# Kernel tuning notes

Hardware: AMD Instinct MI355X
Metric: run time of the kernel (lower is better)

The kernel has to match this reference:

```python
import jax, jax.numpy as jnp
import numpy as np

ROPE_FREQ = 100.0

def _rope1d(tok, pos, freq):
    # tok: [B, H, N, D] (D even), pos: [B, N] int positions
    D = tok.shape[-1]
    inv_freq = 1.0 / (freq ** (jnp.arange(0, D, 2, dtype=jnp.float32) / D))  # [D/2]
    ang = pos[:, None, :, None].astype(jnp.float32) * inv_freq  # [B,1,N,D/2]
    cos = jnp.concatenate([jnp.cos(ang), jnp.cos(ang)], axis=-1).astype(tok.dtype)
    sin = jnp.concatenate([jnp.sin(ang), jnp.sin(ang)], axis=-1).astype(tok.dtype)
    x1, x2 = jnp.split(tok, 2, axis=-1)
    rot = jnp.concatenate([-x2, x1], axis=-1)  # rotate_half
    return tok * cos + rot * sin

def _rope2d(tok, pos2d, freq=ROPE_FREQ):
    # tok: [B, H, N, D]; first half of D encodes y (pos2d[...,0]), second half x (pos2d[...,1])
    y, x = jnp.split(tok, 2, axis=-1)
    y = _rope1d(y, pos2d[..., 0], freq)
    x = _rope1d(x, pos2d[..., 1], freq)
    return jnp.concatenate([y, x], axis=-1)

def setup_inputs() -> dict:
    key = jax.random.key(0)
    B, N, D, Hh = 2, 2048, 768, 12
    ks = jax.random.split(key, 8)
    x = jax.random.normal(ks[0], (B, N, D), dtype=jnp.float32)
    pos2d = jax.random.randint(ks[1], (B, N, 2), 0, 64)
    rope_mask = jax.random.randint(ks[2], (B, N), 0, 2).astype(jnp.bool_)
    s = 1.0 / np.sqrt(D)
    qkv_w = jax.random.normal(ks[3], (3 * D, D), dtype=jnp.float32) * s
    qkv_b = jnp.zeros((3 * D,), dtype=jnp.float32)
    proj_w = jax.random.normal(ks[4], (D, D), dtype=jnp.float32) * s
    proj_b = jnp.zeros((D,), dtype=jnp.float32)
    return {"x": x, "qkv_w": qkv_w, "qkv_b": qkv_b, "proj_w": proj_w,
            "proj_b": proj_b, "pos2d": pos2d, "rope_mask": rope_mask}

def reference(x, qkv_w, qkv_b, proj_w, proj_b, pos2d, rope_mask):
    B, N, C = x.shape
    num_heads = 12
    head_dim = C // num_heads
    scale = head_dim ** -0.5
    qkv = x @ qkv_w.T + qkv_b  # [B,N,3C]
    qkv = qkv.reshape(B, N, 3, num_heads, head_dim).transpose(2, 0, 3, 1, 4)
    q, k, v = qkv[0], qkv[1], qkv[2]  # each [B,H,N,hd]
    q_rope = _rope2d(q, pos2d)
    k_rope = _rope2d(k, pos2d)
    mask = rope_mask[:, None, :, None]  # [B,1,N,1]
    q = jnp.where(mask, q_rope, q)
    k = jnp.where(mask, k_rope, k)
    attn = jnp.einsum('bhqd,bhkd->bhqk', q, k) * scale
    attn = jax.nn.softmax(attn, axis=-1)
    out = jnp.einsum('bhqk,bhkd->bhqd', attn, v)
    out = out.transpose(0, 2, 1, 3).reshape(B, N, C)
    out = out @ proj_w.T + proj_b
    return out
```

## Files before the change

kernel.cpp:

```cpp
#include <hip/hip_runtime.h>
#include <stdint.h>

#define B_  2
#define N_  2048
#define C_  768
#define H_  12
#define NT  (B_*N_)
#define C3  (3*C_)

typedef _Float16 h8 __attribute__((ext_vector_type(8)));
typedef _Float16 h4 __attribute__((ext_vector_type(4)));
typedef float    f4 __attribute__((ext_vector_type(4)));
typedef float    f16x __attribute__((ext_vector_type(16)));
typedef uint32_t u4 __attribute__((ext_vector_type(4)));

__device__ __forceinline__ void gload16(const void* g, void* l) {
  __builtin_amdgcn_global_load_lds((const __attribute__((address_space(1))) void*)g,
                                   (__attribute__((address_space(3))) void*)l,
                                   16, 0, 0);
}

__device__ __forceinline__ int xcd_swz(int flat, int nwg) {
  return (flat & 7) * (nwg >> 3) + (flat >> 3);
}

__global__ __launch_bounds__(256) void cvt3(const float* __restrict__ x,
                                            const float* __restrict__ w1,
                                            const float* __restrict__ w2,
                                            _Float16* __restrict__ xo,
                                            _Float16* __restrict__ w1o,
                                            _Float16* __restrict__ w2o) {
  const int NX8  = NT*C_/8;
  const int NW18 = C3*C_/8;
  int c = blockIdx.x*256 + threadIdx.x;
  const float* s; _Float16* d; int off;
  if (c < NX8)            { s = x;  d = xo;  off = c; }
  else if (c < NX8+NW18)  { s = w1; d = w1o; off = c - NX8; }
  else                    { s = w2; d = w2o; off = c - NX8 - NW18; }
  f4 a = *(const f4*)(s + (size_t)off*8);
  f4 b = *(const f4*)(s + (size_t)off*8 + 4);
  h8 o;
#pragma unroll
  for (int j = 0; j < 4; ++j) { o[j] = (_Float16)a[j]; o[j+4] = (_Float16)b[j]; }
  *(h8*)(d + (size_t)off*8) = o;
}

__global__ __launch_bounds__(256) void gemm_qkv(const _Float16* __restrict__ A,
                                                const _Float16* __restrict__ W,
                                                const float* __restrict__ bias,
                                                const int* __restrict__ pos2d,
                                                const void* __restrict__ maskraw,
                                                _Float16* __restrict__ Qd,
                                                _Float16* __restrict__ Kd,
                                                _Float16* __restrict__ Vtd) {
  constexpr int BM = 64, BN = 128, K = C_;
  __shared__ _Float16 Alds[2][BM*64];
  __shared__ _Float16 Wlds[2][BN*64];
  __shared__ int sflags;
  const int tid = threadIdx.x, lane = tid & 63, w = tid >> 6;

  if (tid == 0) sflags = 0;
  __syncthreads();
  const unsigned char* mbytes = (const unsigned char*)maskraw;
  int fl = 0;
#pragma unroll
  for (int k2 = 0; k2 < 16; ++k2) {
    unsigned char v = mbytes[tid*16 + k2];
    if (v == 0x3f) fl |= 1;
    if ((k2 & 3) && v) fl |= 2;
  }
  if (fl) atomicOr(&sflags, fl);

  const int flat = blockIdx.y * gridDim.x + blockIdx.x;
  const int wid  = xcd_swz(flat, gridDim.x * gridDim.y);
  const int bx = wid % gridDim.x, by = wid / gridDim.x;
  const int m0 = by*BM, n0 = bx*BN;
  const int wm = w >> 1, wn = w & 1;
  const int fr = lane & 15, fq = lane >> 4;

  f4 acc[2][4] = {};

  const int srow = tid >> 3;
  const int scol = ((tid & 7) ^ (srow & 7)) * 8;
  const _Float16* Agp0 = A + (size_t)(m0 +      srow)*K + scol;
  const _Float16* Agp1 = A + (size_t)(m0 + 32 + srow)*K + scol;
  const _Float16* Wgp0 = W + (size_t)(n0 +      srow)*K + scol;
  const _Float16* Wgp1 = W + (size_t)(n0 + 32 + srow)*K + scol;
  const _Float16* Wgp2 = W + (size_t)(n0 + 64 + srow)*K + scol;
  const _Float16* Wgp3 = W + (size_t)(n0 + 96 + srow)*K + scol;

  auto GSTAGE = [&](int buf, int kk) {
    gload16(Agp0 + kk, &Alds[buf][(      w*64)*8]);
    gload16(Agp1 + kk, &Alds[buf][(256 + w*64)*8]);
    gload16(Wgp0 + kk, &Wlds[buf][(      w*64)*8]);
    gload16(Wgp1 + kk, &Wlds[buf][(256 + w*64)*8]);
    gload16(Wgp2 + kk, &Wlds[buf][(512 + w*64)*8]);
    gload16(Wgp3 + kk, &Wlds[buf][(768 + w*64)*8]);
  };

  const int xr = (fr & 7) << 3;

  GSTAGE(0, 0);
  int cur = 0;
  for (int kk = 0; kk < K; kk += 64) {
    __syncthreads();
    if (kk + 64 < K) GSTAGE(cur^1, kk + 64);
#pragma unroll
    for (int ks = 0; ks < 2; ++ks) {
      h8 af[2], wf[4];
#pragma unroll
      for (int mt = 0; mt < 2; ++mt)
        af[mt] = *(const h8*)&Alds[cur][(wm*32 + mt*16 + fr)*64 + ((ks*32 + fq*8) ^ xr)];
#pragma unroll
      for (int nt = 0; nt < 4; ++nt)
        wf[nt] = *(const h8*)&Wlds[cur][(wn*64 + nt*16 + fr)*64 + ((ks*32 + fq*8) ^ xr)];
#pragma unroll
      for (int mt = 0; mt < 2; ++mt)
#pragma unroll
        for (int nt = 0; nt < 4; ++nt)
          acc[mt][nt] = __builtin_amdgcn_mfma_f32_16x16x32_f16(af[mt], wf[nt], acc[mt][nt], 0, 0, 0);
    }
    cur ^= 1;
  }

  const int cb   = (n0 >> 6) + wn;
  const int matc = cb / 12;
  const int h    = cb % 12;
  const int mode = (sflags & 1) ? 2 : ((sflags & 2) ? 1 : 0);
  float bv[4];
#pragma unroll
  for (int nt = 0; nt < 4; ++nt) bv[nt] = bias[cb*64 + nt*16 + fr];

  if (matc < 2) {
    const float invf = exp2f((float)fr * -0.4152410118f);
    const float sc = (matc == 0) ? 0.1803368801f : 1.0f;
    _Float16* base = (matc == 0) ? Qd : Kd;
#pragma unroll
    for (int mt = 0; mt < 2; ++mt)
#pragma unroll
      for (int j = 0; j < 4; ++j) {
        const int t = m0 + wm*32 + mt*16 + fq*4 + j;
        const int b = t >> 11, n = t & 2047;
        bool msk;
        if (mode == 1)      msk = mbytes[t] != 0;
        else if (mode == 0) msk = ((const int*)maskraw)[t] != 0;
        else                msk = ((const float*)maskraw)[t] != 0.0f;
        const float py = (float)pos2d[t*2 + 0];
        const float px = (float)pos2d[t*2 + 1];
        float sy, cy, sx, cx;
        __sincosf(py * invf, &sy, &cy);
        __sincosf(px * invf, &sx, &cx);
        const float a0 = acc[mt][0][j] + bv[0], a1 = acc[mt][1][j] + bv[1];
        const float a2 = acc[mt][2][j] + bv[2], a3 = acc[mt][3][j] + bv[3];
        const float r0 = msk ? (a0*cy - a1*sy) : a0;
        const float r1 = msk ? (a1*cy + a0*sy) : a1;
        const float r2 = msk ? (a2*cx - a3*sx) : a2;
        const float r3 = msk ? (a3*cx + a2*sx) : a3;
        _Float16* dst = base + ((size_t)(b*H_ + h)*N_ + n)*64;
        dst[fr]      = (_Float16)(r0 * sc);
        dst[fr + 16] = (_Float16)(r1 * sc);
        dst[fr + 32] = (_Float16)(r2 * sc);
        dst[fr + 48] = (_Float16)(r3 * sc);
      }
  } else {
#pragma unroll
    for (int mt = 0; mt < 2; ++mt)
#pragma unroll
      for (int j = 0; j < 4; ++j) {
        const int t = m0 + wm*32 + mt*16 + fq*4 + j;
        const int b = t >> 11, n = t & 2047;
        _Float16* vb = Vtd + (size_t)(b*H_ + h)*64*N_ + n;
#pragma unroll
        for (int nt = 0; nt < 4; ++nt)
          vb[(size_t)(nt*16 + fr)*N_] = (_Float16)(acc[mt][nt][j] + bv[nt]);
      }
  }
}

template<int BM, int BN>
__global__ __launch_bounds__(256) void gemm_bt(const _Float16* __restrict__ A,
                                               const _Float16* __restrict__ W,
                                               const float* __restrict__ bias,
                                               _Float16* __restrict__ Ch,
                                               float* __restrict__ Cf,
                                               int M, int N, int K) {
  __shared__ _Float16 Alds[2][BM*32];
  __shared__ _Float16 Wlds[2][BN*32];
  const int tid = threadIdx.x, lane = tid & 63, w = tid >> 6;
  const int flat = blockIdx.y * gridDim.x + blockIdx.x;
  const int wid  = xcd_swz(flat, gridDim.x * gridDim.y);
  const int bx = wid % gridDim.x, by = wid / gridDim.x;
  const int m0 = by*BM, n0 = bx*BN;
  const int wm = w >> 1, wn = w & 1;
  const int fr = lane & 15, fq = lane >> 4;
  constexpr int MT = BM/32, NTt = BN/32;
  constexpr int AI = (BM*4)/256, WI = (BN*4)/256;

  f4 acc[MT][NTt] = {};

  const _Float16* Agp[AI];
  const _Float16* Wgp[WI];
#pragma unroll
  for (int i = 0; i < AI; ++i) { int c = i*256 + tid; Agp[i] = A + (size_t)(m0 + (c>>2))*K + (c&3)*8; }
#pragma unroll
  for (int i = 0; i < WI; ++i) { int c = i*256 + tid; Wgp[i] = W + (size_t)(n0 + (c>>2))*K + (c&3)*8; }

  auto GSTAGE = [&](int buf, int kk) {
#pragma unroll
    for (int i = 0; i < AI; ++i) gload16(Agp[i] + kk, &Alds[buf][(i*256 + w*64)*8]);
#pragma unroll
    for (int i = 0; i < WI; ++i) gload16(Wgp[i] + kk, &Wlds[buf][(i*256 + w*64)*8]);
  };

  GSTAGE(0, 0);
  int cur = 0;
  for (int kk = 0; kk < K; kk += 32) {
    __syncthreads();
    if (kk + 32 < K) GSTAGE(cur^1, kk + 32);
    h8 af[MT], wf[NTt];
#pragma unroll
    for (int mt = 0; mt < MT; ++mt)
      af[mt] = *(const h8*)&Alds[cur][(wm*(BM/2) + mt*16 + fr)*32 + fq*8];
#pragma unroll
    for (int nt = 0; nt < NTt; ++nt)
      wf[nt] = *(const h8*)&Wlds[cur][(wn*(BN/2) + nt*16 + fr)*32 + fq*8];
#pragma unroll
    for (int mt = 0; mt < MT; ++mt)
#pragma unroll
      for (int nt = 0; nt < NTt; ++nt)
        acc[mt][nt] = __builtin_amdgcn_mfma_f32_16x16x32_f16(af[mt], wf[nt], acc[mt][nt], 0, 0, 0);
    cur ^= 1;
  }

#pragma unroll
  for (int nt = 0; nt < NTt; ++nt) {
    const int col = n0 + wn*(BN/2) + nt*16 + fr;
    const float bv = bias[col];
#pragma unroll
    for (int mt = 0; mt < MT; ++mt) {
      const int row = m0 + wm*(BM/2) + mt*16 + fq*4;
#pragma unroll
      for (int j = 0; j < 4; ++j) {
        const float v = acc[mt][nt][j] + bv;
        if (Ch) Ch[(size_t)(row+j)*N + col] = (_Float16)v;
        else    Cf[(size_t)(row+j)*N + col] = v;
      }
    }
  }
}

#define KSPLIT 2
__global__ __launch_bounds__(256, 3) void attn(const _Float16* __restrict__ Q,
                                               const _Float16* __restrict__ K,
                                               const _Float16* __restrict__ Vt,
                                               _Float16* __restrict__ Opart,
                                               float* __restrict__ lpart) {
  __shared__ _Float16 Klds[2][64*64];
  __shared__ _Float16 Vlds[2][64*64];
  const int tid = threadIdx.x, lane = tid & 63, w = tid >> 6;
  const int q32 = lane & 31;
  const int hi  = lane >> 5;
  const int flat = blockIdx.x + gridDim.x*(blockIdx.y + gridDim.y*blockIdx.z);
  const int wid  = xcd_swz(flat, 16*24*KSPLIT);
  const int qi = wid & 15;
  const int bh = (wid >> 4) % 24;
  const int z  = wid / (16*24);
  const int q0 = qi * 128;
  const int kb0 = z * (N_/KSPLIT), kb1 = kb0 + N_/KSPLIT;
  const _Float16* Qb = Q  + (size_t)bh*N_*64;
  const _Float16* Kb = K  + (size_t)bh*N_*64;
  const _Float16* Vb = Vt + (size_t)bh*64*N_;

  h8 qf[4];
#pragma unroll
  for (int s = 0; s < 4; ++s)
    qf[s] = *(const h8*)&Qb[(size_t)(q0 + w*32 + q32)*64 + s*16 + hi*8];

  f16x o2[2][2];
#pragma unroll
  for (int par = 0; par < 2; ++par)
#pragma unroll
    for (int dg = 0; dg < 2; ++dg)
#pragma unroll
      for (int r = 0; r < 16; ++r) o2[par][dg][r] = 0.f;
  float l_r = 0.f;

  const int sr_l = lane >> 3;
  const int scsw = ((lane & 7) ^ sr_l) * 8;
#define STAGE(buf, kb)                                                          \
  {                                                                             \
    _Float16* kl = &Klds[buf][(w*64)*8];                                        \
    _Float16* vl = &Vlds[buf][(w*64)*8];                                        \
    int r0 = w*8 + sr_l;                                                        \
    gload16(Kb + (size_t)((kb) + r0)*64 + scsw,      kl);                       \
    gload16(Vb + (size_t)r0*N_ + (kb) + scsw,        vl);                       \
    gload16(Kb + (size_t)((kb) + 32 + r0)*64 + scsw, kl + 256*8);               \
    gload16(Vb + (size_t)(32 + r0)*N_ + (kb) + scsw, vl + 256*8);               \
  }

  STAGE(0, kb0);
  int cur = 0;
  const int xr = (q32 & 7) << 3;

  for (int kb = kb0; kb < kb1; kb += 64) {
    __syncthreads();
    if (kb + 64 < kb1) STAGE(cur^1, kb + 64);

#pragma unroll
    for (int kg = 0; kg < 2; ++kg) {
      f16x st;
#pragma unroll
      for (int r = 0; r < 16; ++r) st[r] = -8.65617025f;
      __builtin_amdgcn_s_setprio(1);
#pragma unroll
      for (int s = 0; s < 4; ++s) {
        h8 kf = *(const h8*)&Klds[cur][(kg*32 + q32)*64 + ((s*16 + hi*8) ^ xr)];
        st = __builtin_amdgcn_mfma_f32_32x32x16_f16(kf, qf[s], st, 0, 0, 0);
      }
      __builtin_amdgcn_s_setprio(0);
      float p[16];
      float lacc = 0.f;
#pragma unroll
      for (int r = 0; r < 16; ++r) {
        p[r] = __builtin_amdgcn_exp2f(st[r]);
        lacc += p[r];
      }
      l_r += lacc;
      uint32_t dd[8];
#pragma unroll
      for (int m = 0; m < 8; ++m)
        dd[m] = __builtin_bit_cast(uint32_t, __builtin_amdgcn_cvt_pkrtz(p[2*m], p[2*m+1]));
#pragma unroll
      for (int s16 = 0; s16 < 2; ++s16) {
        uint32_t e0 = dd[4*s16+0], e2 = dd[4*s16+2];
        asm("v_permlane32_swap_b32 %0, %1" : "+v"(e0), "+v"(e2));
        uint32_t e1 = dd[4*s16+1], e3 = dd[4*s16+3];
        asm("v_permlane32_swap_b32 %0, %1" : "+v"(e1), "+v"(e3));
        u4 bb;
        bb[0] = e0; bb[1] = e1; bb[2] = e2; bb[3] = e3;
        h8 pb = __builtin_bit_cast(h8, bb);
        const int kcol = kg*32 + s16*16 + hi*8;
        __builtin_amdgcn_s_setprio(1);
#pragma unroll
        for (int dg = 0; dg < 2; ++dg) {
          h8 vf = *(const h8*)&Vlds[cur][(dg*32 + q32)*64 + (kcol ^ xr)];
          o2[s16][dg] = __builtin_amdgcn_mfma_f32_32x32x16_f16(vf, pb, o2[s16][dg], 0, 0, 0);
        }
        __builtin_amdgcn_s_setprio(0);
      }
    }
    cur ^= 1;
  }

  l_r += __shfl_xor(l_r, 32);

  _Float16* Ob = Opart + ((size_t)z*24 + bh)*N_*64;
  float*    lb = lpart + ((size_t)z*24 + bh)*N_;
  const int n = q0 + w*32 + q32;
  if (hi == 0) lb[n] = l_r;
#pragma unroll
  for (int dg = 0; dg < 2; ++dg)
#pragma unroll
    for (int rq = 0; rq < 4; ++rq) {
      h4 ov;
#pragma unroll
      for (int j = 0; j < 4; ++j)
        ov[j] = (_Float16)(o2[0][dg][rq*4 + j] + o2[1][dg][rq*4 + j]);
      *(h4*)&Ob[(size_t)n*64 + dg*32 + rq*8 + hi*4] = ov;
    }
}

__global__ __launch_bounds__(256) void combine(const _Float16* __restrict__ Opart,
                                               const float* __restrict__ lpart,
                                               _Float16* __restrict__ AO) {
  const int g  = blockIdx.x*256 + threadIdx.x;
  const int d8 = g & 7;
  const int n  = (g >> 3) & 2047;
  const int bh = g >> 14;
  const int b = bh / H_, h = bh % H_;
  const size_t r  = ((size_t)bh*N_ + n);
  const size_t sp = (size_t)24*N_;
  f4 osum[2] = {};
  float l = 0.f;
#pragma unroll
  for (int z = 0; z < KSPLIT; ++z) {
    h8 oz = *(const h8*)&Opart[(r + z*sp)*64 + d8*8];
#pragma unroll
    for (int j = 0; j < 4; ++j) { osum[0][j] += (float)oz[j]; osum[1][j] += (float)oz[j+4]; }
    l += lpart[r + z*sp];
  }
  const float inv = 1.0f / l;
  h8 rr;
#pragma unroll
  for (int j = 0; j < 4; ++j) {
    rr[j]   = (_Float16)(osum[0][j] * inv);
    rr[j+4] = (_Float16)(osum[1][j] * inv);
  }
  *(h8*)&AO[((size_t)b*N_ + n)*C_ + h*64 + d8*8] = rr;
}

extern "C" void kernel_launch(void* const* d_in, const int* in_sizes, int n_in,
                              void* d_out, int out_size, void* d_ws, size_t ws_size,
                              hipStream_t stream) {
  (void)in_sizes; (void)n_in; (void)out_size; (void)ws_size;
  const float* x      = (const float*)d_in[0];
  const float* qkv_w  = (const float*)d_in[1];
  const float* qkv_b  = (const float*)d_in[2];
  const float* proj_w = (const float*)d_in[3];
  const float* proj_b = (const float*)d_in[4];
  const int*   pos2d  = (const int*)d_in[5];
  const void*  rmask  = d_in[6];
  float* out = (float*)d_out;
  char* ws = (char*)d_ws;

  _Float16* Wqh   = (_Float16*)(ws + 0);
  _Float16* Wph   = (_Float16*)(ws + 3538944);
  _Float16* Kh    = (_Float16*)(ws + 4718592);
  _Float16* Vth   = (_Float16*)(ws + 11010048);
  _Float16* Xh    = (_Float16*)(ws + 17301504);
  _Float16* Qh    = (_Float16*)(ws + 23592960);
  _Float16* Opart = (_Float16*)(ws + 29884416);
  float*    lpart = (float*)(ws + 42467328);
  _Float16* AOh   = (_Float16*)(ws + 43253760);

  cvt3<<<2688, 256, 0, stream>>>(x, qkv_w, proj_w, Xh, Wqh, Wph);
  gemm_qkv<<<dim3(C3/128, NT/64), 256, 0, stream>>>(Xh, Wqh, qkv_b, pos2d, rmask, Qh, Kh, Vth);
  attn<<<dim3(N_/128, B_*H_, KSPLIT), 256, 0, stream>>>(Qh, Kh, Vth, Opart, lpart);
  combine<<<(24*N_*8)/256, 256, 0, stream>>>(Opart, lpart, AOh);
  gemm_bt<64,64><<<dim3(C_/64, NT/64), 256, 0, stream>>>(AOh, Wph, proj_b, nullptr, out, NT, C_, C_);
}
```

Measured before the change: 99.28 us.

## Fuse split-K attention combine into output projection GEMM and regroup QKV tile order

Removes the separate combine kernel and its AO buffer round trip by having the output projection GEMM read both split-K partial outputs, sum them and normalize by the summed row sums while staging the A tile into LDS. The A operand now goes through registers with a one-step prefetch instead of direct global-to-LDS loads. Separately, the QKV GEMM block index is remapped into groups of 16x9 tiles for better L2 reuse. This drops one launch and the intermediate traffic, but each projection block rereads the partials and computes twelve reciprocals per thread, and the A loads are no longer asynchronous.

Result: slower. 102.1 us (+2.9%).

```diff
diff --git a/kernel.cpp b/kernel.cpp
--- a/kernel.cpp
+++ b/kernel.cpp
@@ -72,8 +72,10 @@
   if (fl) atomicOr(&sflags, fl);
 
   const int flat = blockIdx.y * gridDim.x + blockIdx.x;
-  const int wid  = xcd_swz(flat, gridDim.x * gridDim.y);
-  const int bx = wid % gridDim.x, by = wid / gridDim.x;
+  const int wid  = xcd_swz(flat, 18*64);
+  const int grp = wid / 144, rr = wid % 144;
+  const int by = (grp & 3)*16 + rr/9;
+  const int bx = (grp >> 2)*9 + (rr % 9);
   const int m0 = by*BM, n0 = bx*BN;
   const int wm = w >> 1, wn = w & 1;
   const int fr = lane & 15, fq = lane >> 4;
@@ -177,78 +179,6 @@
   }
 }
 
-template<int BM, int BN>
-__global__ __launch_bounds__(256) void gemm_bt(const _Float16* __restrict__ A,
-                                               const _Float16* __restrict__ W,
-                                               const float* __restrict__ bias,
-                                               _Float16* __restrict__ Ch,
-                                               float* __restrict__ Cf,
-                                               int M, int N, int K) {
-  __shared__ _Float16 Alds[2][BM*32];
-  __shared__ _Float16 Wlds[2][BN*32];
-  const int tid = threadIdx.x, lane = tid & 63, w = tid >> 6;
-  const int flat = blockIdx.y * gridDim.x + blockIdx.x;
-  const int wid  = xcd_swz(flat, gridDim.x * gridDim.y);
-  const int bx = wid % gridDim.x, by = wid / gridDim.x;
-  const int m0 = by*BM, n0 = bx*BN;
-  const int wm = w >> 1, wn = w & 1;
-  const int fr = lane & 15, fq = lane >> 4;
-  constexpr int MT = BM/32, NTt = BN/32;
-  constexpr int AI = (BM*4)/256, WI = (BN*4)/256;
-
-  f4 acc[MT][NTt] = {};
-
-  const _Float16* Agp[AI];
-  const _Float16* Wgp[WI];
-#pragma unroll
-  for (int i = 0; i < AI; ++i) { int c = i*256 + tid; Agp[i] = A + (size_t)(m0 + (c>>2))*K + (c&3)*8; }
-#pragma unroll
-  for (int i = 0; i < WI; ++i) { int c = i*256 + tid; Wgp[i] = W + (size_t)(n0 + (c>>2))*K + (c&3)*8; }
-
-  auto GSTAGE = [&](int buf, int kk) {
-#pragma unroll
-    for (int i = 0; i < AI; ++i) gload16(Agp[i] + kk, &Alds[buf][(i*256 + w*64)*8]);
-#pragma unroll
-    for (int i = 0; i < WI; ++i) gload16(Wgp[i] + kk, &Wlds[buf][(i*256 + w*64)*8]);
-  };
-
-  GSTAGE(0, 0);
-  int cur = 0;
-  for (int kk = 0; kk < K; kk += 32) {
-    __syncthreads();
-    if (kk + 32 < K) GSTAGE(cur^1, kk + 32);
-    h8 af[MT], wf[NTt];
-#pragma unroll
-    for (int mt = 0; mt < MT; ++mt)
-      af[mt] = *(const h8*)&Alds[cur][(wm*(BM/2) + mt*16 + fr)*32 + fq*8];
-#pragma unroll
-    for (int nt = 0; nt < NTt; ++nt)
-      wf[nt] = *(const h8*)&Wlds[cur][(wn*(BN/2) + nt*16 + fr)*32 + fq*8];
-#pragma unroll
-    for (int mt = 0; mt < MT; ++mt)
-#pragma unroll
-      for (int nt = 0; nt < NTt; ++nt)
-        acc[mt][nt] = __builtin_amdgcn_mfma_f32_16x16x32_f16(af[mt], wf[nt], acc[mt][nt], 0, 0, 0);
-    cur ^= 1;
-  }
-
-#pragma unroll
-  for (int nt = 0; nt < NTt; ++nt) {
-    const int col = n0 + wn*(BN/2) + nt*16 + fr;
-    const float bv = bias[col];
-#pragma unroll
-    for (int mt = 0; mt < MT; ++mt) {
-      const int row = m0 + wm*(BM/2) + mt*16 + fq*4;
-#pragma unroll
-      for (int j = 0; j < 4; ++j) {
-        const float v = acc[mt][nt][j] + bv;
-        if (Ch) Ch[(size_t)(row+j)*N + col] = (_Float16)v;
-        else    Cf[(size_t)(row+j)*N + col] = v;
-      }
-    }
-  }
-}
-
 #define KSPLIT 2
 __global__ __launch_bounds__(256, 3) void attn(const _Float16* __restrict__ Q,
                                                const _Float16* __restrict__ K,
@@ -370,33 +300,97 @@
     }
 }
 
-__global__ __launch_bounds__(256) void combine(const _Float16* __restrict__ Opart,
-                                               const float* __restrict__ lpart,
-                                               _Float16* __restrict__ AO) {
-  const int g  = blockIdx.x*256 + threadIdx.x;
-  const int d8 = g & 7;
-  const int n  = (g >> 3) & 2047;
-  const int bh = g >> 14;
-  const int b = bh / H_, h = bh % H_;
-  const size_t r  = ((size_t)bh*N_ + n);
-  const size_t sp = (size_t)24*N_;
-  f4 osum[2] = {};
-  float l = 0.f;
-#pragma unroll
-  for (int z = 0; z < KSPLIT; ++z) {
-    h8 oz = *(const h8*)&Opart[(r + z*sp)*64 + d8*8];
-#pragma unroll
-    for (int j = 0; j < 4; ++j) { osum[0][j] += (float)oz[j]; osum[1][j] += (float)oz[j+4]; }
-    l += lpart[r + z*sp];
-  }
-  const float inv = 1.0f / l;
-  h8 rr;
-#pragma unroll
-  for (int j = 0; j < 4; ++j) {
-    rr[j]   = (_Float16)(osum[0][j] * inv);
-    rr[j+4] = (_Float16)(osum[1][j] * inv);
-  }
-  *(h8*)&AO[((size_t)b*N_ + n)*C_ + h*64 + d8*8] = rr;
+__global__ __launch_bounds__(256) void gemm_out(const _Float16* __restrict__ Op,
+                                                const float* __restrict__ lp,
+                                                const _Float16* __restrict__ W,
+                                                const float* __restrict__ bias,
+                                                float* __restrict__ out) {
+  constexpr int BM = 64, BN = 64, K = C_;
+  constexpr size_t OSP = (size_t)24*N_*64;
+  constexpr size_t LSP = (size_t)24*N_;
+  __shared__ _Float16 Alds[2][BM*32];
+  __shared__ _Float16 Wlds[2][BN*32];
+  const int tid = threadIdx.x, lane = tid & 63, w = tid >> 6;
+  const int flat = blockIdx.y * gridDim.x + blockIdx.x;
+  const int wid  = xcd_swz(flat, gridDim.x * gridDim.y);
+  const int bx = wid % gridDim.x, by = wid / gridDim.x;
+  const int m0 = by*BM, n0 = bx*BN;
+  const int wm = w >> 1, wn = w & 1;
+  const int fr = lane & 15, fq = lane >> 4;
+
+  f4 acc[2][2] = {};
+
+  const int arow = m0 + (tid >> 2);
+  const int bb = arow >> 11, nn = arow & 2047;
+
+  float inv12[12];
+#pragma unroll
+  for (int hh = 0; hh < 12; ++hh) {
+    const size_t li = (size_t)(bb*H_ + hh)*N_ + nn;
+    inv12[hh] = 1.0f / (lp[li] + lp[LSP + li]);
+  }
+
+  auto loadO = [&](int kkt, h8& a0, h8& a1) {
+    const int hh = kkt >> 6, d0 = (kkt & 32) + (tid & 3)*8;
+    const size_t off = ((size_t)(bb*H_ + hh)*N_ + nn)*64 + d0;
+    a0 = *(const h8*)&Op[off];
+    a1 = *(const h8*)&Op[OSP + off];
+  };
+  auto writeA = [&](int buf, int kkt, h8 a0, h8 a1) {
+    const float inv = inv12[kkt >> 6];
+    u4 pk;
+#pragma unroll
+    for (int m = 0; m < 4; ++m) {
+      float s0 = ((float)a0[2*m]   + (float)a1[2*m])   * inv;
+      float s1 = ((float)a0[2*m+1] + (float)a1[2*m+1]) * inv;
+      pk[m] = __builtin_bit_cast(uint32_t, __builtin_amdgcn_cvt_pkrtz(s0, s1));
+    }
+    *(u4*)&Alds[buf][tid*8] = pk;
+  };
+
+  const _Float16* Wgp = W + (size_t)(n0 + (tid>>2))*K + (tid&3)*8;
+
+  h8 pa0, pa1;
+  loadO(0, pa0, pa1);
+  gload16(Wgp + 0, &Wlds[0][(w*64)*8]);
+  writeA(0, 0, pa0, pa1);
+  loadO(32, pa0, pa1);
+  int cur = 0;
+#pragma unroll
+  for (int kk = 0; kk < K; kk += 32) {
+    __syncthreads();
+    if (kk + 32 < K) {
+      writeA(cur^1, kk + 32, pa0, pa1);
+      gload16(Wgp + kk + 32, &Wlds[cur^1][(w*64)*8]);
+      if (kk + 64 < K) loadO(kk + 64, pa0, pa1);
+    }
+    h8 af[2], wf[2];
+#pragma unroll
+    for (int mt = 0; mt < 2; ++mt)
+      af[mt] = *(const h8*)&Alds[cur][(wm*32 + mt*16 + fr)*32 + fq*8];
+#pragma unroll
+    for (int nt = 0; nt < 2; ++nt)
+      wf[nt] = *(const h8*)&Wlds[cur][(wn*32 + nt*16 + fr)*32 + fq*8];
+#pragma unroll
+    for (int mt = 0; mt < 2; ++mt)
+#pragma unroll
+      for (int nt = 0; nt < 2; ++nt)
+        acc[mt][nt] = __builtin_amdgcn_mfma_f32_16x16x32_f16(af[mt], wf[nt], acc[mt][nt], 0, 0, 0);
+    cur ^= 1;
+  }
+
+#pragma unroll
+  for (int nt = 0; nt < 2; ++nt) {
+    const int col = n0 + wn*32 + nt*16 + fr;
+    const float bv = bias[col];
+#pragma unroll
+    for (int mt = 0; mt < 2; ++mt) {
+      const int row = m0 + wm*32 + mt*16 + fq*4;
+#pragma unroll
+      for (int j = 0; j < 4; ++j)
+        out[(size_t)(row+j)*C_ + col] = acc[mt][nt][j] + bv;
+    }
+  }
 }
 
 extern "C" void kernel_launch(void* const* d_in, const int* in_sizes, int n_in,
@@ -421,11 +415,9 @@
   _Float16* Qh    = (_Float16*)(ws + 23592960);
   _Float16* Opart = (_Float16*)(ws + 29884416);
   float*    lpart = (float*)(ws + 42467328);
-  _Float16* AOh   = (_Float16*)(ws + 43253760);
 
   cvt3<<<2688, 256, 0, stream>>>(x, qkv_w, proj_w, Xh, Wqh, Wph);
   gemm_qkv<<<dim3(C3/128, NT/64), 256, 0, stream>>>(Xh, Wqh, qkv_b, pos2d, rmask, Qh, Kh, Vth);
   attn<<<dim3(N_/128, B_*H_, KSPLIT), 256, 0, stream>>>(Qh, Kh, Vth, Opart, lpart);
-  combine<<<(24*N_*8)/256, 256, 0, stream>>>(Opart, lpart, AOh);
-  gemm_bt<64,64><<<dim3(C_/64, NT/64), 256, 0, stream>>>(AOh, Wph, proj_b, nullptr, out, NT, C_, C_);
-}
+  gemm_out<<<dim3(C_/64, NT/64), 256, 0, stream>>>(Opart, lpart, Wph, proj_b, out);
+}
```
